# Performance work log

Measured on AMD Instinct MI355X. Metric: run time of the kernel, lower is better.

The kernel has to match this reference:

```python
import jax, jax.numpy as jnp
import numpy as np

B, N, X, Y, Z = 1, 64, 256, 256, 32
THRESHOLD = 0.5  # default forward kwarg


def setup_inputs() -> dict:
    key = jax.random.key(0)
    # 0/1 float masks, as the module expects ('boolean tensors with values 0 and 1')
    u = jax.random.uniform(key, (B, N, X, Y, Z), dtype=jnp.float32)
    mask = (u < 0.3).astype(jnp.float32)
    return {"mask": mask}


def reference(mask):
    n = mask.shape[1]
    flat = mask.reshape(n, -1)          # [N, V], values in {0, 1}
    score = flat.sum(-1)                # per-instance voxel count (torch: reshape(...).sum(-1))
    # For 0/1 masks: count((a+b)>1) == a.b  and  count((a+b)>0) == |a|+|b|-a.b
    inter = flat @ flat.T               # [N, N] pairwise intersection counts
    union = score[:, None] + score[None, :] - inter
    iou = jax.lax.stop_gradient(inter / union)   # suppression logic is non-differentiable
    s = jax.lax.stop_gradient(score)

    def outer(i, ind):
        active = ind[i] > 0  # torch: 'if ind[i] == 0: continue'

        def cond(c):
            j, _, done = c
            return (j < n) & (~done)

        def body(c):
            j, ind, _ = c
            hit = iou[i, j] > THRESHOLD
            # if iou > thr and score[j] > score[i]: ind[i] = 0 (no break)
            ind = ind.at[i].set(jnp.where(hit & (s[j] > s[i]), 0, ind[i]))
            # if iou > thr and score[i] > score[j]: ind[j] = 0; break
            sup_j = hit & (s[i] > s[j])
            ind = ind.at[j].set(jnp.where(sup_j, 0, ind[j]))
            return (j + 1, ind, sup_j)

        _, ind, _ = jax.lax.while_loop(cond, body, (jnp.int32(0), ind, ~active))
        return ind

    ind = jax.lax.fori_loop(0, n, outer, jnp.ones(n, dtype=jnp.int32))
    return ind > 0
```

## Files before the change

kernel.cpp:

```cpp
#include <hip/hip_runtime.h>


#define NROWS          64
#define ROWLEN         2097152u
#define CHUNK_FLOATS   2048
#define NCHUNKS        65536
#define WORDS_PER_ROW  65536
#define NPAIRS         2080
#define K2_BLOCKS      256
#define WPC            256

__global__ __launch_bounds__(256) void nms_pack(const unsigned int* __restrict__ mask,
                                                unsigned int* __restrict__ packed) {
    const int lane = threadIdx.x & 63;
    const int wv   = threadIdx.x >> 6;
    const unsigned int wave_id = blockIdx.x * 4 + wv;
    for (int it = 0; it < 16; ++it) {
        const size_t c = (size_t)wave_id * 16 + it;
        const unsigned int* base = mask + c * CHUNK_FLOATS + lane * 4;
        unsigned int word = 0u;
        #pragma unroll
        for (int k = 0; k < 8; ++k) {
            const uint4 v = *(const uint4*)(base + k * 256);
            word |= (v.x != 0u ? 1u : 0u) << (k * 4 + 0);
            word |= (v.y != 0u ? 1u : 0u) << (k * 4 + 1);
            word |= (v.z != 0u ? 1u : 0u) << (k * 4 + 2);
            word |= (v.w != 0u ? 1u : 0u) << (k * 4 + 3);
        }
        packed[c * 64 + lane] = word;
    }
}

__global__ __launch_bounds__(256) void nms_pairs(const unsigned int* __restrict__ packed,
                                                 unsigned int* __restrict__ partial) {
    __shared__ unsigned int tile[NROWS * WPC];
    const int tid = threadIdx.x;
    const int b   = blockIdx.x;

    const uint4* p4 = (const uint4*)packed;
    uint4*       t4 = (uint4*)tile;
    for (int q = tid; q < NROWS * (WPC / 4); q += 256) {
        const int r  = q >> 6;
        const int w4 = q & 63;
        t4[q] = p4[(size_t)r * (WORDS_PER_ROW / 4) + (size_t)b * (WPC / 4) + w4];
    }
    __syncthreads();

    const unsigned long long* t64 = (const unsigned long long*)tile;
    const int lane = tid & 63;
    for (int p = tid; p < NPAIRS; p += 256) {
        int rem = p, i = 0;
        while (rem >= 64 - i) { rem -= 64 - i; ++i; }
        const int j = i + rem;
        const unsigned long long* ri = t64 + i * (WPC / 2);
        const unsigned long long* rj = t64 + j * (WPC / 2);
        unsigned int acc = 0;
        #pragma unroll 8
        for (int w = 0; w < WPC / 2; ++w) {
            const int m = (w + lane) & (WPC / 2 - 1);
            acc += (unsigned int)__popcll(ri[m] & rj[m]);
        }
        partial[(size_t)p * K2_BLOCKS + b] = acc;
    }
}

__global__ __launch_bounds__(256) void nms_reduce(const unsigned int* __restrict__ partial,
                                                  unsigned int* __restrict__ inter) {
    const int p    = blockIdx.x * 4 + (threadIdx.x >> 6);
    const int lane = threadIdx.x & 63;
    const uint4 v = ((const uint4*)partial)[(size_t)p * 64 + lane];
    unsigned int s = v.x + v.y + v.z + v.w;
    #pragma unroll
    for (int off = 32; off >= 1; off >>= 1) s += (unsigned int)__shfl_xor((int)s, off);
    if (lane == 0) inter[p] = s;
}

__global__ __launch_bounds__(256) void nms_select(const unsigned int* __restrict__ inter,
                                                  int* __restrict__ out) {
    __shared__ unsigned int sI[NPAIRS];
    const int tid = threadIdx.x;
    for (int p = tid; p < NPAIRS; p += 256) sI[p] = inter[p];
    __syncthreads();
    if (tid < 64) {
        const int j = tid;
        unsigned int cnt[64];
        #pragma unroll
        for (int i = 0; i < 64; ++i) {
            const int lo = i < j ? i : j, hi = i < j ? j : i;
            cnt[i] = sI[lo * 64 - lo * (lo - 1) / 2 + (hi - lo)];
        }
        const unsigned int s = cnt[j];
        int ind = 1;
        #pragma unroll
        for (int i = 0; i < 64; ++i) {
            const int          ind_i = __shfl(ind, i);
            const unsigned int s_i   = (unsigned int)__shfl((int)s, i);
            const unsigned int ov    = cnt[i];
            const unsigned int uni   = s_i + s - ov;
            const bool hit = (2u * ov > uni);
            const unsigned long long A = __ballot(hit && (s > s_i));
            const unsigned long long B = __ballot(hit && (s_i > s));
            if (ind_i) {
                const int jb = B ? (__ffsll((unsigned long long)B) - 1) : 64;
                const unsigned long long low = (jb >= 64) ? ~0ULL : ((1ULL << jb) - 1ULL);
                if ((A & low) && j == i) ind = 0;
                if (jb < 64 && j == jb) ind = 0;
            }
        }
        out[j] = ind;
    }
}

extern "C" void kernel_launch(void* const* d_in, const int* in_sizes, int n_in,
                              void* d_out, int out_size, void* d_ws, size_t ws_size,
                              hipStream_t stream) {
    const unsigned int* mask = (const unsigned int*)d_in[0];
    int* out = (int*)d_out;

    unsigned int* packed  = (unsigned int*)d_ws;
    unsigned int* partial = packed + (size_t)NCHUNKS * 64;
    unsigned int* inter   = partial + (size_t)NPAIRS * K2_BLOCKS;

    nms_pack  <<<1024, 256, 0, stream>>>(mask, packed);
    nms_pairs <<<K2_BLOCKS, 256, 0, stream>>>(packed, partial);
    nms_reduce<<<NPAIRS / 4, 256, 0, stream>>>(partial, inter);
    nms_select<<<1, 256, 0, stream>>>(inter, out);
}
```

Measured before the change: 750.1 us.

## Fuse mask bit-packing with pairwise popcount using register-tiled 4x4 row blocks

```diff
diff --git a/kernel.cpp b/kernel.cpp
--- a/kernel.cpp
+++ b/kernel.cpp
@@ -1,23 +1,25 @@
 #include <hip/hip_runtime.h>
 
 
-#define NROWS          64
-#define ROWLEN         2097152u
-#define CHUNK_FLOATS   2048
-#define NCHUNKS        65536
-#define WORDS_PER_ROW  65536
-#define NPAIRS         2080
-#define K2_BLOCKS      256
-#define WPC            256
+#define NROWS   64
+#define ROWLEN  2097152u
+#define NB      1024
+#define CHUNK   2048
+#define NPAIRS  2080
+#define NPART   (NB * 2)
 
-__global__ __launch_bounds__(256) void nms_pack(const unsigned int* __restrict__ mask,
-                                                unsigned int* __restrict__ packed) {
-    const int lane = threadIdx.x & 63;
-    const int wv   = threadIdx.x >> 6;
-    const unsigned int wave_id = blockIdx.x * 4 + wv;
-    for (int it = 0; it < 16; ++it) {
-        const size_t c = (size_t)wave_id * 16 + it;
-        const unsigned int* base = mask + c * CHUNK_FLOATS + lane * 4;
+__global__ __launch_bounds__(256, 4) void nms_fused(const unsigned int* __restrict__ mask,
+                                                    unsigned int* __restrict__ partial) {
+    __shared__ unsigned int bits32[NROWS][64];
+    const int tid  = threadIdx.x;
+    const int lane = tid & 63;
+    const int wv   = tid >> 6;
+    const size_t colbase = (size_t)blockIdx.x * CHUNK;
+
+    #pragma unroll 2
+    for (int rr = 0; rr < 16; ++rr) {
+        const int r = wv * 16 + rr;
+        const unsigned int* base = mask + (size_t)r * ROWLEN + colbase + lane * 4;
         unsigned int word = 0u;
         #pragma unroll
         for (int k = 0; k < 8; ++k) {
@@ -27,40 +29,50 @@
             word |= (v.z != 0u ? 1u : 0u) << (k * 4 + 2);
             word |= (v.w != 0u ? 1u : 0u) << (k * 4 + 3);
         }
-        packed[c * 64 + lane] = word;
-    }
-}
-
-__global__ __launch_bounds__(256) void nms_pairs(const unsigned int* __restrict__ packed,
-                                                 unsigned int* __restrict__ partial) {
-    __shared__ unsigned int tile[NROWS * WPC];
-    const int tid = threadIdx.x;
-    const int b   = blockIdx.x;
-
-    const uint4* p4 = (const uint4*)packed;
-    uint4*       t4 = (uint4*)tile;
-    for (int q = tid; q < NROWS * (WPC / 4); q += 256) {
-        const int r  = q >> 6;
-        const int w4 = q & 63;
-        t4[q] = p4[(size_t)r * (WORDS_PER_ROW / 4) + (size_t)b * (WPC / 4) + w4];
+        bits32[r][lane] = word;
     }
     __syncthreads();
 
-    const unsigned long long* t64 = (const unsigned long long*)tile;
-    const int lane = tid & 63;
-    for (int p = tid; p < NPAIRS; p += 256) {
-        int rem = p, i = 0;
-        while (rem >= 64 - i) { rem -= 64 - i; ++i; }
-        const int j = i + rem;
-        const unsigned long long* ri = t64 + i * (WPC / 2);
-        const unsigned long long* rj = t64 + j * (WPC / 2);
-        unsigned int acc = 0;
-        #pragma unroll 8
-        for (int w = 0; w < WPC / 2; ++w) {
-            const int m = (w + lane) & (WPC / 2 - 1);
-            acc += (unsigned int)__popcll(ri[m] & rj[m]);
+    for (int item = tid; item < 272; item += 256) {
+        const int h = item & 1;
+        int rem = item >> 1, gi = 0;
+        while (rem >= 16 - gi) { rem -= 16 - gi; ++gi; }
+        const int gj = gi + rem;
+
+        unsigned int acc[4][4];
+        #pragma unroll
+        for (int a = 0; a < 4; ++a)
+            #pragma unroll
+            for (int b = 0; b < 4; ++b) acc[a][b] = 0u;
+
+        #pragma unroll 4
+        for (int step = 0; step < 16; ++step) {
+            const int w = h * 16 + ((step + lane) & 15);
+            unsigned long long ai[4], bj[4];
+            #pragma unroll
+            for (int k = 0; k < 4; ++k)
+                ai[k] = ((const unsigned long long*)bits32[gi * 4 + k])[w];
+            #pragma unroll
+            for (int k = 0; k < 4; ++k)
+                bj[k] = ((const unsigned long long*)bits32[gj * 4 + k])[w];
+            #pragma unroll
+            for (int a = 0; a < 4; ++a)
+                #pragma unroll
+                for (int b = 0; b < 4; ++b)
+                    acc[a][b] += (unsigned int)__popcll(ai[a] & bj[b]);
         }
-        partial[(size_t)p * K2_BLOCKS + b] = acc;
+
+        const size_t sbase = ((size_t)blockIdx.x * 2 + h) * NPAIRS;
+        #pragma unroll
+        for (int a = 0; a < 4; ++a) {
+            const int i = gi * 4 + a;
+            #pragma unroll
+            for (int b = 0; b < 4; ++b) {
+                const int j = gj * 4 + b;
+                if (i <= j)
+                    partial[sbase + (i * 64 - i * (i - 1) / 2 + (j - i))] = acc[a][b];
+            }
+        }
     }
 }
 
@@ -68,8 +80,10 @@
                                                   unsigned int* __restrict__ inter) {
     const int p    = blockIdx.x * 4 + (threadIdx.x >> 6);
     const int lane = threadIdx.x & 63;
-    const uint4 v = ((const uint4*)partial)[(size_t)p * 64 + lane];
-    unsigned int s = v.x + v.y + v.z + v.w;
+    unsigned int s = 0;
+    #pragma unroll 8
+    for (int it = 0; it < NPART / 64; ++it)
+        s += partial[(size_t)(it * 64 + lane) * NPAIRS + p];
     #pragma unroll
     for (int off = 32; off >= 1; off >>= 1) s += (unsigned int)__shfl_xor((int)s, off);
     if (lane == 0) inter[p] = s;
@@ -117,12 +131,10 @@
     const unsigned int* mask = (const unsigned int*)d_in[0];
     int* out = (int*)d_out;
 
-    unsigned int* packed  = (unsigned int*)d_ws;
-    unsigned int* partial = packed + (size_t)NCHUNKS * 64;
-    unsigned int* inter   = partial + (size_t)NPAIRS * K2_BLOCKS;
+    unsigned int* partial = (unsigned int*)d_ws;
+    unsigned int* inter   = partial + (size_t)NPART * NPAIRS;
 
-    nms_pack  <<<1024, 256, 0, stream>>>(mask, packed);
-    nms_pairs <<<K2_BLOCKS, 256, 0, stream>>>(packed, partial);
+    nms_fused <<<NB, 256, 0, stream>>>(mask, partial);
     nms_reduce<<<NPAIRS / 4, 256, 0, stream>>>(partial, inter);
     nms_select<<<1, 256, 0, stream>>>(inter, out);
 }
```

New measurement: 715.9 us. -4.6%, faster.
